# Performance work log

Measured on AMD Instinct MI355X. Metric: run time of the kernel, lower is better.

Reference implementation:

```python
import jax, jax.numpy as jnp
import numpy as np

D_MODEL = 2048
NUM_HEADS = 16
HEAD_DIM = D_MODEL // NUM_HEADS


def setup_inputs() -> dict:
    key = jax.random.key(0)
    ks = jax.random.split(key, 9)
    B, S, D = 2, 2048, D_MODEL
    scale = 1.0 / np.sqrt(D)
    x = jax.random.normal(ks[0], (B, S, D), dtype=jnp.float32)
    # torch nn.Linear weights are [out, in]; y = x @ W.T + b
    wq = jax.random.normal(ks[1], (D, D), dtype=jnp.float32) * scale
    wk = jax.random.normal(ks[2], (D, D), dtype=jnp.float32) * scale
    wv = jax.random.normal(ks[3], (D, D), dtype=jnp.float32) * scale
    wo = jax.random.normal(ks[4], (D, D), dtype=jnp.float32) * scale
    bq = jax.random.normal(ks[5], (D,), dtype=jnp.float32) * scale
    bk = jax.random.normal(ks[6], (D,), dtype=jnp.float32) * scale
    bv = jax.random.normal(ks[7], (D,), dtype=jnp.float32) * scale
    bo = jax.random.normal(ks[8], (D,), dtype=jnp.float32) * scale
    return {"x": x, "wq": wq, "bq": bq, "wk": wk, "bk": bk,
            "wv": wv, "bv": bv, "wo": wo, "bo": bo}


def reference(x, wq, bq, wk, bk, wv, bv, wo, bo):
    B, S, D = x.shape
    H, Dh = NUM_HEADS, HEAD_DIM
    # projections (torch Linear: x @ W.T + b), reshape to [B, H, S, Dh]
    q = (x @ wq.T + bq).reshape(B, S, H, Dh).transpose(0, 2, 1, 3)
    k = (x @ wk.T + bk).reshape(B, S, H, Dh).transpose(0, 2, 1, 3)
    v = (x @ wv.T + bv).reshape(B, S, H, Dh).transpose(0, 2, 1, 3)
    scores = jnp.einsum("bhqd,bhkd->bhqk", q, k) / jnp.sqrt(jnp.float32(Dh))
    attn = jax.nn.softmax(scores, axis=-1)
    out = jnp.einsum("bhqk,bhkd->bhqd", attn, v)  # [B, H, S, Dh]
    out = out.transpose(0, 2, 1, 3).reshape(B, S, D)
    return out @ wo.T + bo
```

## Files before the change

kernel.cpp:

```cpp
#include <hip/hip_runtime.h>

#define DEV __device__ __forceinline__

typedef __attribute__((ext_vector_type(8))) short bf16x8;
typedef __attribute__((ext_vector_type(4))) float f32x4;

constexpr int D_MODEL = 2048;
constexpr int NHEAD = 16;
constexpr int DH = 128;
constexpr int SS = 2048;
constexpr int KK = 2048;

DEV unsigned short f2bf(float f) {
  unsigned int u = __builtin_bit_cast(unsigned int, f);
  u = (u + 0x7fff + ((u >> 16) & 1)) >> 16;
  return (unsigned short)u;
}

DEV void async16(const void* g, void* l) {
  __builtin_amdgcn_global_load_lds(
      (const __attribute__((address_space(1))) unsigned int*)g,
      (__attribute__((address_space(3))) unsigned int*)l, 16, 0, 0);
}

DEV f32x4 mfma16(bf16x8 a, bf16x8 b, f32x4 c) {
  return __builtin_amdgcn_mfma_f32_16x16x32_bf16(a, b, c, 0, 0, 0);
}

DEV float exp2f_raw(float x) {
  float y;
  asm("v_exp_f32 %0, %1" : "=v"(y) : "v"(x));
  return y;
}

__global__ __launch_bounds__(256) void cast_all(
    const float* __restrict__ x, const float* __restrict__ wq,
    const float* __restrict__ wk, const float* __restrict__ wv,
    const float* __restrict__ wo, unsigned short* __restrict__ xb,
    unsigned short* __restrict__ wb) {
  long i4 = ((long)blockIdx.x * 256 + threadIdx.x) * 4;
  const float* src;
  unsigned short* dst;
  long off;
  if (i4 < 8388608) {
    src = x; dst = xb; off = i4;
  } else {
    long j = i4 - 8388608;
    int seg = (int)(j >> 22);
    off = j & 4194303;
    src = (seg == 0) ? wq : (seg == 1) ? wk : (seg == 2) ? wv : wo;
    dst = wb + ((long)seg << 22);
  }
  float4 v = *(const float4*)(src + off);
  ushort4 u;
  u.x = f2bf(v.x); u.y = f2bf(v.y); u.z = f2bf(v.z); u.w = f2bf(v.w);
  *(ushort4*)(dst + off) = u;
}

template <int MODE>
__global__ __launch_bounds__(256, 2) void gemm_bt(
    const unsigned short* __restrict__ A, const unsigned short* __restrict__ W,
    const float* __restrict__ b0, const float* __restrict__ b1,
    const float* __restrict__ b2, unsigned short* __restrict__ oq,
    unsigned short* __restrict__ ok, unsigned short* __restrict__ ov,
    float* __restrict__ of) {
  __shared__ unsigned short lA[128 * 32];
  __shared__ unsigned short lB[128 * 32];
  const int t = threadIdx.x;
  const int lane = t & 63, wid = t >> 6;
  const int m0 = blockIdx.y * 128, n0 = blockIdx.x * 128;
  const int srow = t >> 2, scol = (t & 3) * 8;
  const unsigned short* ga = A + (long)(m0 + srow) * KK + scol;
  const unsigned short* gw = W + (long)(n0 + srow) * KK + scol;
  const int i16 = lane & 15, g4 = lane >> 4;
  const int wr = wid >> 1, wc = wid & 1;
  f32x4 acc[4][4] = {};
  for (int k0 = 0; k0 < KK; k0 += 32) {
    async16(ga + k0, &lA[wid * 512]);
    async16(ga + 64 * KK + k0, &lA[2048 + wid * 512]);
    async16(gw + k0, &lB[wid * 512]);
    async16(gw + 64 * KK + k0, &lB[2048 + wid * 512]);
    __syncthreads();
    bf16x8 af[4], bfr[4];
#pragma unroll
    for (int i = 0; i < 4; i++)
      af[i] = *(const bf16x8*)&lA[(wr * 64 + i * 16 + i16) * 32 + g4 * 8];
#pragma unroll
    for (int j = 0; j < 4; j++)
      bfr[j] = *(const bf16x8*)&lB[(wc * 64 + j * 16 + i16) * 32 + g4 * 8];
#pragma unroll
    for (int i = 0; i < 4; i++)
#pragma unroll
      for (int j = 0; j < 4; j++) acc[i][j] = mfma16(af[i], bfr[j], acc[i][j]);
    __syncthreads();
  }
#pragma unroll
  for (int i = 0; i < 4; i++) {
#pragma unroll
    for (int j = 0; j < 4; j++) {
      const int ng = n0 + wc * 64 + j * 16 + i16;
#pragma unroll
      for (int r = 0; r < 4; r++) {
        const int mg = m0 + wr * 64 + i * 16 + g4 * 4 + r;
        float v = acc[i][j][r];
        if (MODE == 1) {
          v += b0[ng];
          of[(long)mg * D_MODEL + ng] = v;
        } else {
          const int seg = ng >> 11, n = ng & 2047;
          const int h = n >> 7, d = n & 127;
          const int b_ = mg >> 11, s_ = mg & 2047;
          const long bh = b_ * NHEAD + h;
          if (seg == 0) {
            v = (v + b0[n]) * (0.08838834764831845f * 1.4426950408889634f);
            oq[(bh * SS + s_) * DH + d] = f2bf(v);
          } else if (seg == 1) {
            v += b1[n];
            ok[(bh * SS + s_) * DH + d] = f2bf(v);
          } else {
            v += b2[n];
            ov[(bh * DH + d) * SS + s_] = f2bf(v);
          }
        }
      }
    }
  }
}

__global__ __launch_bounds__(256, 2) void attn_fwd(
    const unsigned short* __restrict__ Q, const unsigned short* __restrict__ Kb,
    const unsigned short* __restrict__ Vt, unsigned short* __restrict__ Ob) {
  __shared__ unsigned short lK[2][64 * 128];
  __shared__ unsigned short lV[2][128 * 64];
  __shared__ unsigned short lP[4][16 * 64];
  const int t = threadIdx.x, lane = t & 63, wid = t >> 6;
  const int i16 = lane & 15, g4 = lane >> 4;
  const int qt = blockIdx.x, bh = blockIdx.y;
  bf16x8 qa[2][4];
#pragma unroll
  for (int qi = 0; qi < 2; qi++) {
    const long qrow = (long)bh * SS + qt * 128 + wid * 32 + qi * 16 + i16;
#pragma unroll
    for (int ks = 0; ks < 4; ks++)
      qa[qi][ks] = *(const bf16x8*)&Q[qrow * DH + ks * 32 + g4 * 8];
  }
  bf16x8 vones;
#pragma unroll
  for (int j = 0; j < 8; j++) vones[j] = (short)0x3F80;
  f32x4 o[2][8] = {};
  f32x4 ol[2] = {};
  float mrow[2][4] = {{-1e30f, -1e30f, -1e30f, -1e30f},
                      {-1e30f, -1e30f, -1e30f, -1e30f}};
  const char* kbase = (const char*)(Kb + (long)bh * SS * DH);
  const char* vbase = (const char*)(Vt + (long)bh * DH * SS);

  auto STAGE = [&](int buf, int kv0) {
#pragma unroll
    for (int r = 0; r < 4; r++) {
      const int o_ = r * 4096 + t * 16;
      const int okk = o_ ^ (((o_ >> 8) & 7) << 4);
      async16(kbase + (long)kv0 * 256 + okk,
              (char*)lK + buf * 16384 + r * 4096 + wid * 1024);
      const int vrow = o_ >> 7;
      const int inr = (o_ ^ ((vrow & 7) << 4)) & 127;
      async16(vbase + (long)vrow * (SS * 2) + kv0 * 2 + inr,
              (char*)lV + buf * 16384 + r * 4096 + wid * 1024);
    }
  };

  STAGE(0, 0);
  asm volatile("s_waitcnt vmcnt(0)");
  __syncthreads();
  int cur = 0;
  for (int it = 0; it < SS / 64; ++it) {
    if (it + 1 < SS / 64) STAGE(cur ^ 1, (it + 1) * 64);
    const char* kb = (const char*)lK + cur * 16384;
    const char* vb = (const char*)lV + cur * 16384;
    f32x4 s4[2][4] = {};
    __builtin_amdgcn_s_setprio(1);
#pragma unroll
    for (int kc = 0; kc < 4; kc++) {
      const int row = kc * 16 + i16;
#pragma unroll
      for (int ks = 0; ks < 4; ks++) {
        const int lb = row * 256 + ((ks * 64 + g4 * 16) ^ ((row & 7) << 4));
        bf16x8 kf = *(const bf16x8*)(kb + lb);
        s4[0][kc] = mfma16(qa[0][ks], kf, s4[0][kc]);
        s4[1][kc] = mfma16(qa[1][ks], kf, s4[1][kc]);
      }
    }
    __builtin_amdgcn_s_setprio(0);
#pragma unroll
    for (int qi = 0; qi < 2; qi++) {
      float mx[4];
#pragma unroll
      for (int r = 0; r < 4; r++) {
        float m_ = fmaxf(fmaxf(s4[qi][0][r], s4[qi][1][r]),
                         fmaxf(s4[qi][2][r], s4[qi][3][r]));
        m_ = fmaxf(m_, __shfl_xor(m_, 1));
        m_ = fmaxf(m_, __shfl_xor(m_, 2));
        m_ = fmaxf(m_, __shfl_xor(m_, 4));
        m_ = fmaxf(m_, __shfl_xor(m_, 8));
        mx[r] = m_;
      }
      const int ok = (mx[0] <= mrow[qi][0] + 8.f) &
                     (mx[1] <= mrow[qi][1] + 8.f) &
                     (mx[2] <= mrow[qi][2] + 8.f) &
                     (mx[3] <= mrow[qi][3] + 8.f);
      if (!__all(ok)) {
#pragma unroll
        for (int r = 0; r < 4; r++) {
          const float mnew = fmaxf(mrow[qi][r], mx[r]);
          const float fac = exp2f_raw(mrow[qi][r] - mnew);
          mrow[qi][r] = mnew;
          ol[qi][r] *= fac;
#pragma unroll
          for (int df = 0; df < 8; df++) o[qi][df][r] *= fac;
        }
      }
#pragma unroll
      for (int kc = 0; kc < 4; kc++)
#pragma unroll
        for (int r = 0; r < 4; r++)
          s4[qi][kc][r] = exp2f_raw(s4[qi][kc][r] - mrow[qi][r]);
    }
    bf16x8 pa[2][2];
#pragma unroll
    for (int qi = 0; qi < 2; qi++) {
#pragma unroll
      for (int r = 0; r < 4; r++) {
        const int prow = g4 * 4 + r;
        const int swz = (prow & 7) << 4;
#pragma unroll
        for (int kc = 0; kc < 4; kc++) {
          const int col = kc * 16 + i16;
          *(unsigned short*)((char*)&lP[wid][0] + prow * 128 +
                             ((col * 2) ^ swz)) = f2bf(s4[qi][kc][r]);
        }
      }
#pragma unroll
      for (int ks = 0; ks < 2; ks++) {
        const int lb = i16 * 128 + ((ks * 64 + g4 * 16) ^ ((i16 & 7) << 4));
        pa[qi][ks] = *(const bf16x8*)((const char*)&lP[wid][0] + lb);
      }
    }
    __builtin_amdgcn_s_setprio(1);
#pragma unroll
    for (int ks = 0; ks < 2; ks++) {
      ol[0] = mfma16(pa[0][ks], vones, ol[0]);
      ol[1] = mfma16(pa[1][ks], vones, ol[1]);
    }
#pragma unroll
    for (int df = 0; df < 8; df++) {
#pragma unroll
      for (int ks = 0; ks < 2; ks++) {
        const int row = df * 16 + i16;
        const int lb = row * 128 + ((ks * 64 + g4 * 16) ^ ((row & 7) << 4));
        bf16x8 vf = *(const bf16x8*)(vb + lb);
        o[0][df] = mfma16(pa[0][ks], vf, o[0][df]);
        o[1][df] = mfma16(pa[1][ks], vf, o[1][df]);
      }
    }
    __builtin_amdgcn_s_setprio(0);
    asm volatile("s_waitcnt vmcnt(0)");
    __syncthreads();
    cur ^= 1;
  }
  const int b_ = bh >> 4, h = bh & 15;
#pragma unroll
  for (int qi = 0; qi < 2; qi++) {
    float inv[4];
#pragma unroll
    for (int r = 0; r < 4; r++) inv[r] = __builtin_amdgcn_rcpf(ol[qi][r]);
#pragma unroll
    for (int df = 0; df < 8; df++) {
#pragma unroll
      for (int r = 0; r < 4; r++) {
        const float v = o[qi][df][r] * inv[r];
        const long mg =
            (long)b_ * SS + qt * 128 + wid * 32 + qi * 16 + g4 * 4 + r;
        Ob[mg * D_MODEL + h * DH + df * 16 + i16] = f2bf(v);
      }
    }
  }
}

extern "C" void kernel_launch(void* const* d_in, const int* in_sizes, int n_in,
                              void* d_out, int out_size, void* d_ws,
                              size_t ws_size, hipStream_t stream) {
  const float* x = (const float*)d_in[0];
  const float* wq = (const float*)d_in[1];
  const float* bq = (const float*)d_in[2];
  const float* wk = (const float*)d_in[3];
  const float* bk = (const float*)d_in[4];
  const float* wv = (const float*)d_in[5];
  const float* bv = (const float*)d_in[6];
  const float* wo = (const float*)d_in[7];
  const float* bo = (const float*)d_in[8];
  char* ws = (char*)d_ws;
  unsigned short* xb = (unsigned short*)(ws);
  unsigned short* wb = (unsigned short*)(ws + (16l << 20));
  unsigned short* wob = (unsigned short*)(ws + (40l << 20));
  unsigned short* Qb = (unsigned short*)(ws + (48l << 20));
  unsigned short* Kbf = (unsigned short*)(ws + (64l << 20));
  unsigned short* Vtb = (unsigned short*)(ws + (80l << 20));
  unsigned short* Atb = (unsigned short*)(ws);

  cast_all<<<24576, 256, 0, stream>>>(x, wq, wk, wv, wo, xb, wb);
  gemm_bt<0><<<dim3(48, 32), 256, 0, stream>>>(xb, wb, bq, bk, bv, Qb, Kbf,
                                               Vtb, nullptr);
  attn_fwd<<<dim3(16, 32), 256, 0, stream>>>(Qb, Kbf, Vtb, Atb);
  gemm_bt<1><<<dim3(16, 32), 256, 0, stream>>>(
      Atb, wob, bo, nullptr, nullptr, nullptr, nullptr, nullptr,
      (float*)d_out);
}
```

Baseline: 456.8 us.

## Stage QKV epilogue through LDS for coalesced stores; widen attention blocks to 512 threads

The QKV projection epilogue now writes bf16 results into a padded LDS tile, transposing it for V, and then emits 16-byte coalesced stores to the Q/K/Vt head layouts instead of scattered 2-byte stores. The attention kernel uses 512-thread blocks covering 256 query rows, so each staged K/V tile is shared by twice as many waves and global K/V traffic halves. In exchange the QKV GEMM uses about 34KB more LDS, which may cut occupancy, and the attention grid shrinks to 256 blocks, which may leave some CUs idle.

```diff
diff --git a/kernel.cpp b/kernel.cpp
--- a/kernel.cpp
+++ b/kernel.cpp
@@ -66,6 +66,8 @@
     float* __restrict__ of) {
   __shared__ unsigned short lA[128 * 32];
   __shared__ unsigned short lB[128 * 32];
+  constexpr int LCS = (MODE == 0) ? 128 * 136 : 16;
+  __shared__ __align__(16) unsigned short lC[LCS];
   const int t = threadIdx.x;
   const int lane = t & 63, wid = t >> 6;
   const int m0 = blockIdx.y * 128, n0 = blockIdx.x * 128;
@@ -94,52 +96,76 @@
       for (int j = 0; j < 4; j++) acc[i][j] = mfma16(af[i], bfr[j], acc[i][j]);
     __syncthreads();
   }
-#pragma unroll
-  for (int i = 0; i < 4; i++) {
-#pragma unroll
-    for (int j = 0; j < 4; j++) {
-      const int ng = n0 + wc * 64 + j * 16 + i16;
-#pragma unroll
-      for (int r = 0; r < 4; r++) {
-        const int mg = m0 + wr * 64 + i * 16 + g4 * 4 + r;
-        float v = acc[i][j][r];
-        if (MODE == 1) {
-          v += b0[ng];
-          of[(long)mg * D_MODEL + ng] = v;
-        } else {
-          const int seg = ng >> 11, n = ng & 2047;
-          const int h = n >> 7, d = n & 127;
-          const int b_ = mg >> 11, s_ = mg & 2047;
-          const long bh = b_ * NHEAD + h;
+  if (MODE == 1) {
+#pragma unroll
+    for (int i = 0; i < 4; i++) {
+#pragma unroll
+      for (int j = 0; j < 4; j++) {
+        const int ng = n0 + wc * 64 + j * 16 + i16;
+#pragma unroll
+        for (int r = 0; r < 4; r++) {
+          const int mg = m0 + wr * 64 + i * 16 + g4 * 4 + r;
+          of[(long)mg * D_MODEL + ng] = acc[i][j][r] + b0[ng];
+        }
+      }
+    }
+  } else {
+    const int seg = n0 >> 11;
+    const int h0 = (n0 & 2047) >> 7;
+    const int b_ = m0 >> 11;
+    const int s0_ = m0 & 2047;
+#pragma unroll
+    for (int i = 0; i < 4; i++) {
+#pragma unroll
+      for (int j = 0; j < 4; j++) {
+        const int nl = wc * 64 + j * 16 + i16;
+        const int n = (n0 & 2047) + nl;
+#pragma unroll
+        for (int r = 0; r < 4; r++) {
+          const int ml = wr * 64 + i * 16 + g4 * 4 + r;
+          float v = acc[i][j][r];
           if (seg == 0) {
             v = (v + b0[n]) * (0.08838834764831845f * 1.4426950408889634f);
-            oq[(bh * SS + s_) * DH + d] = f2bf(v);
+            lC[ml * 136 + nl] = f2bf(v);
           } else if (seg == 1) {
-            v += b1[n];
-            ok[(bh * SS + s_) * DH + d] = f2bf(v);
+            lC[ml * 136 + nl] = f2bf(v + b1[n]);
           } else {
-            v += b2[n];
-            ov[(bh * DH + d) * SS + s_] = f2bf(v);
+            lC[nl * 136 + ml] = f2bf(v + b2[n]);
           }
         }
       }
     }
-  }
-}
-
-__global__ __launch_bounds__(256, 2) void attn_fwd(
+    __syncthreads();
+#pragma unroll
+    for (int rep = 0; rep < 8; rep++) {
+      const int idx = rep * 256 + t;
+      const int row = idx >> 4, c16 = idx & 15;
+      const bf16x8 v8 = *(const bf16x8*)&lC[row * 136 + c16 * 8];
+      if (seg == 2) {
+        *(bf16x8*)&ov[((long)(b_ * NHEAD + h0) * DH + row) * SS + s0_ +
+                      c16 * 8] = v8;
+      } else {
+        unsigned short* base = (seg == 0) ? oq : ok;
+        *(bf16x8*)&base[((long)(b_ * NHEAD + h0) * SS + (s0_ + row)) * DH +
+                        c16 * 8] = v8;
+      }
+    }
+  }
+}
+
+__global__ __launch_bounds__(512, 2) void attn_fwd(
     const unsigned short* __restrict__ Q, const unsigned short* __restrict__ Kb,
     const unsigned short* __restrict__ Vt, unsigned short* __restrict__ Ob) {
   __shared__ unsigned short lK[2][64 * 128];
   __shared__ unsigned short lV[2][128 * 64];
-  __shared__ unsigned short lP[4][16 * 64];
+  __shared__ unsigned short lP[8][16 * 64];
   const int t = threadIdx.x, lane = t & 63, wid = t >> 6;
   const int i16 = lane & 15, g4 = lane >> 4;
   const int qt = blockIdx.x, bh = blockIdx.y;
   bf16x8 qa[2][4];
 #pragma unroll
   for (int qi = 0; qi < 2; qi++) {
-    const long qrow = (long)bh * SS + qt * 128 + wid * 32 + qi * 16 + i16;
+    const long qrow = (long)bh * SS + qt * 256 + wid * 32 + qi * 16 + i16;
 #pragma unroll
     for (int ks = 0; ks < 4; ks++)
       qa[qi][ks] = *(const bf16x8*)&Q[qrow * DH + ks * 32 + g4 * 8];
@@ -156,15 +182,15 @@
 
   auto STAGE = [&](int buf, int kv0) {
 #pragma unroll
-    for (int r = 0; r < 4; r++) {
-      const int o_ = r * 4096 + t * 16;
+    for (int r = 0; r < 2; r++) {
+      const int o_ = r * 8192 + t * 16;
       const int okk = o_ ^ (((o_ >> 8) & 7) << 4);
       async16(kbase + (long)kv0 * 256 + okk,
-              (char*)lK + buf * 16384 + r * 4096 + wid * 1024);
+              (char*)lK + buf * 16384 + r * 8192 + wid * 1024);
       const int vrow = o_ >> 7;
       const int inr = (o_ ^ ((vrow & 7) << 4)) & 127;
       async16(vbase + (long)vrow * (SS * 2) + kv0 * 2 + inr,
-              (char*)lV + buf * 16384 + r * 4096 + wid * 1024);
+              (char*)lV + buf * 16384 + r * 8192 + wid * 1024);
     }
   };
 
@@ -278,7 +304,7 @@
       for (int r = 0; r < 4; r++) {
         const float v = o[qi][df][r] * inv[r];
         const long mg =
-            (long)b_ * SS + qt * 128 + wid * 32 + qi * 16 + g4 * 4 + r;
+            (long)b_ * SS + qt * 256 + wid * 32 + qi * 16 + g4 * 4 + r;
         Ob[mg * D_MODEL + h * DH + df * 16 + i16] = f2bf(v);
       }
     }
@@ -309,7 +335,7 @@
   cast_all<<<24576, 256, 0, stream>>>(x, wq, wk, wv, wo, xb, wb);
   gemm_bt<0><<<dim3(48, 32), 256, 0, stream>>>(xb, wb, bq, bk, bv, Qb, Kbf,
                                                Vtb, nullptr);
-  attn_fwd<<<dim3(16, 32), 256, 0, stream>>>(Qb, Kbf, Vtb, Atb);
+  attn_fwd<<<dim3(8, 32), 512, 0, stream>>>(Qb, Kbf, Vtb, Atb);
   gemm_bt<1><<<dim3(16, 32), 256, 0, stream>>>(
       Atb, wob, bo, nullptr, nullptr, nullptr, nullptr, nullptr,
       (float*)d_out);
```

Measured after the change: 425.7 us. 1.07x faster.
